# Kernel tuning notes

Hardware: AMD Instinct MI355X
Metric: run time of the kernel (lower is better)

Reference implementation:

```python
import math
import jax, jax.numpy as jnp
import numpy as np

B, T = 4, 160000
D, H, DH, FF, L = 768, 12, 64, 3072, 12
NB, MD = 320, 800  # rel-pos buckets / max distance
CONV = [(1,512,10,5),(512,512,3,2),(512,512,3,2),(512,512,3,2),(512,512,3,2),(512,512,2,2),(512,512,2,2)]
STRIDES = [5,2,2,2,2,2,2]

def _frames(t):
    for _,_,k,s in CONV:
        t = (t - k)//s + 1
    return t
S = _frames(T)  # 499


def setup_inputs() -> dict:
    key = jax.random.key(0)
    ks = iter(jax.random.split(key, 64))
    r = lambda *sh: jax.random.normal(next(ks), sh, jnp.float32) * 0.02
    return {
        "source": jax.random.normal(next(ks), (B, T), jnp.float32),
        "conv_w0": r(512,1,10),
        "conv_w14": r(4,512,512,3),
        "conv_w56": r(2,512,512,2),
        "conv_ln_g": jnp.ones((7,512), jnp.float32), "conv_ln_b": jnp.zeros((7,512), jnp.float32),
        "feat_ln_g": jnp.ones((512,), jnp.float32), "feat_ln_b": jnp.zeros((512,), jnp.float32),
        "proj_w": r(D,512), "proj_b": jnp.zeros((D,), jnp.float32),
        "pos_conv_w": r(D, D//16, 128), "pos_conv_b": jnp.zeros((D,), jnp.float32),
        "enc_ln_g": jnp.ones((D,), jnp.float32), "enc_ln_b": jnp.zeros((D,), jnp.float32),
        "Wq": r(L,D,D), "bq": jnp.zeros((L,D), jnp.float32),
        "Wk": r(L,D,D), "bk": jnp.zeros((L,D), jnp.float32),
        "Wv": r(L,D,D), "bv": jnp.zeros((L,D), jnp.float32),
        "Wo": r(L,D,D), "bo": jnp.zeros((L,D), jnp.float32),
        "grep_w": r(L,8,DH), "grep_b": jnp.zeros((L,8), jnp.float32),
        "grep_a": jnp.ones((L,H), jnp.float32),
        "ln1_g": jnp.ones((L,D), jnp.float32), "ln1_b": jnp.zeros((L,D), jnp.float32),
        "fc1_w": r(L,FF,D), "fc1_b": jnp.zeros((L,FF), jnp.float32),
        "fc2_w": r(L,D,FF), "fc2_b": jnp.zeros((L,D), jnp.float32),
        "ln2_g": jnp.ones((L,D), jnp.float32), "ln2_b": jnp.zeros((L,D), jnp.float32),
        "rel_emb": r(NB,H),
    }


def _ln(x, g, b, eps=1e-5):
    m = jnp.mean(x, -1, keepdims=True)
    v = jnp.mean((x - m) ** 2, -1, keepdims=True)
    return (x - m) * jax.lax.rsqrt(v + eps) * g + b


def _conv1d(x, w, stride, pad=0, groups=1):
    return jax.lax.conv_general_dilated(x, w, (stride,), [(pad, pad)],
        dimension_numbers=('NCH', 'OIH', 'NCH'), feature_group_count=groups)


def _buckets(s):
    # T5-style bidirectional relative-position bucketization (WavLM compute_bias)
    rel = jnp.arange(s)[None, :] - jnp.arange(s)[:, None]  # memory - context
    nb = NB // 2
    b = (rel > 0).astype(jnp.int32) * nb
    n = jnp.abs(rel)
    max_exact = nb // 2
    large = max_exact + (jnp.log(jnp.maximum(n, 1).astype(jnp.float32) / max_exact)
                         / math.log(MD / max_exact) * (nb - max_exact)).astype(jnp.int32)
    large = jnp.minimum(large, nb - 1)
    return b + jnp.where(n < max_exact, n, large)


def _fwd(p):
    # ---- conv feature extractor: (B,T) -> (B,512,S)
    x = p["source"][:, None, :]
    ws = [p["conv_w0"]] + [p["conv_w14"][i] for i in range(4)] + [p["conv_w56"][i] for i in range(2)]
    for i, (w, st) in enumerate(zip(ws, STRIDES)):
        x = _conv1d(x, w, st)
        x = _ln(x.transpose(0, 2, 1), p["conv_ln_g"][i], p["conv_ln_b"][i]).transpose(0, 2, 1)
        x = jax.nn.gelu(x, approximate=False)
    x = x.transpose(0, 2, 1)                       # (B,S,512)
    x = _ln(x, p["feat_ln_g"], p["feat_ln_b"])
    x = x @ p["proj_w"].T + p["proj_b"]            # (B,S,768) post_extract_proj
    # ---- positional conv (kernel 128, pad 64, groups 16, SamePad drops last)
    xc = _conv1d(x.transpose(0, 2, 1), p["pos_conv_w"], 1, pad=64, groups=16) + p["pos_conv_b"][None, :, None]
    xc = jax.nn.gelu(xc[:, :, :-1], approximate=False)
    x = x + xc.transpose(0, 2, 1)
    x = _ln(x, p["enc_ln_g"], p["enc_ln_b"])       # layer_norm_first=False -> LN before layers
    Bn, s, _ = x.shape
    pos_bias = p["rel_emb"][_buckets(s)].transpose(2, 0, 1)  # (H,S,S), computed at layer 0, reused
    scaling = DH ** -0.5
    for l in range(L):
        # gated relative-position bias: gates from raw layer-input split into heads (WavLM fast path)
        ql = x.reshape(Bn, s, H, DH).transpose(0, 2, 1, 3)        # (B,H,S,dh)
        g = jax.nn.sigmoid((jnp.einsum('bhsd,gd->bhsg', ql, p["grep_w"][l]) + p["grep_b"][l])
                           .reshape(Bn, H, s, 2, 4).sum(-1))       # (B,H,S,2)
        gate = g[..., 0] * (g[..., 1] * p["grep_a"][l][None, :, None] - 1.0) + 2.0  # (B,H,S)
        bias = gate[..., None] * pos_bias[None]                    # (B,H,S,S)
        def proj(W, bb):
            return (x @ W.T + bb).reshape(Bn, s, H, DH).transpose(0, 2, 1, 3)
        q = proj(p["Wq"][l], p["bq"][l]) * scaling
        k = proj(p["Wk"][l], p["bk"][l])
        v = proj(p["Wv"][l], p["bv"][l])
        attn = jax.nn.softmax(jnp.einsum('bhsd,bhtd->bhst', q, k) + bias, axis=-1)
        ctx = jnp.einsum('bhst,bhtd->bhsd', attn, v).transpose(0, 2, 1, 3).reshape(Bn, s, D)
        x = _ln(x + ctx @ p["Wo"][l].T + p["bo"][l], p["ln1_g"][l], p["ln1_b"][l])
        h = jax.nn.gelu(x @ p["fc1_w"][l].T + p["fc1_b"][l], approximate=False)
        x = _ln(x + h @ p["fc2_w"][l].T + p["fc2_b"][l], p["ln2_g"][l], p["ln2_b"][l])
    return x


def reference(source, conv_w0, conv_w14, conv_w56, conv_ln_g, conv_ln_b, feat_ln_g, feat_ln_b,
              proj_w, proj_b, pos_conv_w, pos_conv_b, enc_ln_g, enc_ln_b,
              Wq, bq, Wk, bk, Wv, bv, Wo, bo, grep_w, grep_b, grep_a,
              ln1_g, ln1_b, fc1_w, fc1_b, fc2_w, fc2_b, ln2_g, ln2_b, rel_emb):
    p = dict(source=source, conv_w0=conv_w0, conv_w14=conv_w14, conv_w56=conv_w56,
             conv_ln_g=conv_ln_g, conv_ln_b=conv_ln_b, feat_ln_g=feat_ln_g, feat_ln_b=feat_ln_b,
             proj_w=proj_w, proj_b=proj_b, pos_conv_w=pos_conv_w, pos_conv_b=pos_conv_b,
             enc_ln_g=enc_ln_g, enc_ln_b=enc_ln_b, Wq=Wq, bq=bq, Wk=Wk, bk=bk, Wv=Wv, bv=bv,
             Wo=Wo, bo=bo, grep_w=grep_w, grep_b=grep_b, grep_a=grep_a,
             ln1_g=ln1_g, ln1_b=ln1_b, fc1_w=fc1_w, fc1_b=fc1_b, fc2_w=fc2_w, fc2_b=fc2_b,
             ln2_g=ln2_g, ln2_b=ln2_b, rel_emb=rel_emb)
    return _fwd(p)
```

## Files before the change

kernel.cpp:

```cpp
#include <hip/hip_runtime.h>
#include <hip/hip_bf16.h>
#include <math.h>

namespace {

constexpr int BATCH  = 4;
constexpr int T_IN   = 160000;
constexpr int DMODEL = 768;
constexpr int NHEAD  = 12;
constexpr int DHEAD  = 64;
constexpr int FFN    = 3072;
constexpr int NLAYER = 12;
constexpr int SEQ    = 499;
constexpr int SP     = 512;
constexpr int NREL   = 2 * SEQ - 1;

typedef __hip_bfloat16 bf16;
using f32x4 = __attribute__((ext_vector_type(4))) float;
using s16x8 = __attribute__((ext_vector_type(8))) short;

__device__ __forceinline__ float gelu_f(float x){
  return 0.5f * x * (1.0f + erff(x * 0.70710678118654752f));
}

__device__ __forceinline__ unsigned f2bf_rne(float f){
  unsigned u = __float_as_uint(f);
  return (u + 0x7FFFu + ((u >> 16) & 1u)) >> 16;
}

__global__ void fill_f32_kernel(float* __restrict__ out, int n, float val){
  int i = blockIdx.x * 256 + threadIdx.x;
  if (i < n) out[i] = val;
}

__global__ void f2bf_kernel(const float* __restrict__ in, bf16* __restrict__ out, int n){
  int i = blockIdx.x * 256 + threadIdx.x;
  if (i < n) out[i] = __float2bfloat16(in[i]);
}

__global__ void castw6(const float* __restrict__ wq, const float* __restrict__ wk,
                       const float* __restrict__ wv, const float* __restrict__ wo,
                       const float* __restrict__ f1, const float* __restrict__ f2,
                       bf16* __restrict__ d0, bf16* __restrict__ d1, bf16* __restrict__ d2,
                       bf16* __restrict__ d3, bf16* __restrict__ d4, bf16* __restrict__ d5){
  int z = blockIdx.y;
  int idx = blockIdx.x * 256 + threadIdx.x;
  const float* s; bf16* d; int n;
  switch (z){
    case 0: s = wq; d = d0; n = 589824; break;
    case 1: s = wk; d = d1; n = 589824; break;
    case 2: s = wv; d = d2; n = 589824; break;
    case 3: s = wo; d = d3; n = 589824; break;
    case 4: s = f1; d = d4; n = 2359296; break;
    default: s = f2; d = d5; n = 2359296; break;
  }
  if (idx < n) d[idx] = __float2bfloat16(s[idx]);
}

template<int KW>
__global__ void pack_convw(const float* __restrict__ w, bf16* __restrict__ dst){
  int idx = blockIdx.x * 256 + threadIdx.x;
  if (idx >= KW * 512 * 512) return;
  int ci = idx & 511, co = (idx >> 9) & 511, k = idx >> 18;
  dst[idx] = __float2bfloat16(w[((size_t)co * 512 + ci) * KW + k]);
}

__global__ void conv0_kernel(const float* __restrict__ src, const float* __restrict__ w,
                             float* __restrict__ out, int Lout){
  int idx = blockIdx.x * 256 + threadIdx.x;
  if (idx >= 512 * Lout) return;
  int c = idx / Lout, t = idx - c * Lout;
  const float* wr = w + c * 10;
  const float* s  = src + t * 5;
  float acc = 0.f;
#pragma unroll
  for (int k = 0; k < 10; k++) acc += wr[k] * s[k];
  out[idx] = acc;
}

template<int BFOUT>
__global__ void ln_gelu_ch2_kernel(float* __restrict__ x, bf16* __restrict__ ob,
                                   const float* __restrict__ g, const float* __restrict__ b,
                                   int Lt){
  const int tid = threadIdx.x;
  const int tt = tid & 31, tc = tid >> 5;
  const int t = blockIdx.x * 32 + tt;
  __shared__ float sred[8][33], qred[8][33];
  __shared__ float mrow[32], rrow[32];
  float s = 0.f, q = 0.f;
  if (t < Lt){
    const float* xc = x + (size_t)(tc * 64) * Lt + t;
#pragma unroll 8
    for (int j = 0; j < 64; j++){ float v = xc[(size_t)j * Lt]; s += v; q += v * v; }
  }
  sred[tc][tt] = s; qred[tc][tt] = q; __syncthreads();
  if (tid < 32){
    float ss = 0.f, qq = 0.f;
#pragma unroll
    for (int c = 0; c < 8; c++){ ss += sred[c][tid]; qq += qred[c][tid]; }
    float m = ss * (1.f / 512.f);
    float var = qq * (1.f / 512.f) - m * m;
    mrow[tid] = m; rrow[tid] = rsqrtf(var + 1e-5f);
  }
  __syncthreads();
  if (t < Lt){
    float m = mrow[tt], rs = rrow[tt];
    float* xc = x + (size_t)(tc * 64) * Lt + t;
#pragma unroll 8
    for (int j = 0; j < 64; j++){
      int c = tc * 64 + j;
      float v = gelu_f((xc[(size_t)j * Lt] - m) * rs * g[c] + b[c]);
      if (BFOUT) ob[(size_t)c * Lt + t] = __float2bfloat16(v);
      else       xc[(size_t)j * Lt] = v;
    }
  }
}

template<int KW>
__global__ void conv_mfma_kernel(const bf16* __restrict__ in, const bf16* __restrict__ wpk,
                                 float* __restrict__ out, int Lin, int Lout, int outLd){
  __shared__ unsigned comb[130][33];
  __shared__ bf16 As[KW][64][40];
  const int tid = threadIdx.x, wid = tid >> 6, lane = tid & 63;
  const int co0 = blockIdx.x * 64, t0 = blockIdx.y * 128;
  const int wm = (wid >> 1) * 32, wn = (wid & 1) * 64;
  const int fr = lane & 15, fk = (lane >> 4) * 8;
  const int wco = tid >> 2, wci = (tid & 3) * 8;
  f32x4 acc[2][4] = {};
  for (int ci0 = 0; ci0 < 512; ci0 += 32){
#pragma unroll
    for (int k = 0; k < KW; k++)
      *reinterpret_cast<uint4*>(&As[k][wco][wci]) =
        *reinterpret_cast<const uint4*>(&wpk[(size_t)k * 262144 + (size_t)(co0 + wco) * 512 + ci0 + wci]);
    for (int idx = tid; idx < 4096; idx += 256){
      int jp = idx & 127, ci = idx >> 7;
      int gp = t0 * 2 + 2 * jp;
      const bf16* rp = in + (size_t)(ci0 + ci) * Lin;
      unsigned pr = 0;
      if (gp + 1 < Lin) pr = *reinterpret_cast<const unsigned*>(&rp[gp]);
      else if (gp < Lin) pr = *reinterpret_cast<const unsigned short*>(&rp[gp]);
      comb[jp][ci] = pr;
    }
    if (tid < 64){
      int jp = 128 + (tid >> 5), ci = tid & 31;
      int gp = t0 * 2 + 2 * jp;
      const bf16* rp = in + (size_t)(ci0 + ci) * Lin;
      unsigned pr = 0;
      if (gp + 1 < Lin) pr = *reinterpret_cast<const unsigned*>(&rp[gp]);
      else if (gp < Lin) pr = *reinterpret_cast<const unsigned short*>(&rp[gp]);
      comb[jp][ci] = pr;
    }
    __syncthreads();
#pragma unroll
    for (int k = 0; k < KW; k++){
      const int ro = k >> 1, par = k & 1;
      s16x8 a0 = *reinterpret_cast<const s16x8*>(&As[k][wm + fr][fk]);
      s16x8 a1 = *reinterpret_cast<const s16x8*>(&As[k][wm + 16 + fr][fk]);
#pragma unroll
      for (int ni = 0; ni < 4; ni++){
        const unsigned* cp = &comb[wn + ni * 16 + fr + ro][fk];
        unsigned u0 = cp[0], u1 = cp[1], u2 = cp[2], u3 = cp[3];
        unsigned u4 = cp[4], u5 = cp[5], u6 = cp[6], u7 = cp[7];
        uint4 pb;
        if (par){
          pb.x = (u0 >> 16) | (u1 & 0xFFFF0000u);
          pb.y = (u2 >> 16) | (u3 & 0xFFFF0000u);
          pb.z = (u4 >> 16) | (u5 & 0xFFFF0000u);
          pb.w = (u6 >> 16) | (u7 & 0xFFFF0000u);
        } else {
          pb.x = (u0 & 0xFFFFu) | (u1 << 16);
          pb.y = (u2 & 0xFFFFu) | (u3 << 16);
          pb.z = (u4 & 0xFFFFu) | (u5 << 16);
          pb.w = (u6 & 0xFFFFu) | (u7 << 16);
        }
        s16x8 bb = *reinterpret_cast<s16x8*>(&pb);
        acc[0][ni] = __builtin_amdgcn_mfma_f32_16x16x32_bf16(a0, bb, acc[0][ni], 0, 0, 0);
        acc[1][ni] = __builtin_amdgcn_mfma_f32_16x16x32_bf16(a1, bb, acc[1][ni], 0, 0, 0);
      }
    }
    __syncthreads();
  }
  const int cc = lane & 15, crr = (lane >> 4) * 4;
#pragma unroll
  for (int mi = 0; mi < 2; mi++){
#pragma unroll
    for (int ni = 0; ni < 4; ni++){
      int t = t0 + wn + ni * 16 + cc;
      if (t >= Lout) continue;
#pragma unroll
      for (int r = 0; r < 4; r++){
        int co = co0 + wm + mi * 16 + crr + r;
        out[(size_t)co * outLd + t] = acc[mi][ni][r];
      }
    }
  }
}

__global__ void featln_transpose_kernel(const float* __restrict__ xin,
                                        const float* __restrict__ g, const float* __restrict__ b,
                                        float* __restrict__ feat){
  int t = blockIdx.x * 256 + threadIdx.x;
  if (t >= SEQ) return;
  float s = 0.f, sq = 0.f;
  for (int c = 0; c < 512; c++){ float v = xin[c * SEQ + t]; s += v; sq += v * v; }
  float m = s * (1.f / 512.f), var = sq * (1.f / 512.f) - m * m, rs = rsqrtf(var + 1e-5f);
  for (int c = 0; c < 512; c++)
    feat[t * 512 + c] = (xin[c * SEQ + t] - m) * rs * g[c] + b[c];
}

template<int ACT>
__global__ void gemm_mfma_f32(const float* __restrict__ A, const float* __restrict__ W,
                              const float* __restrict__ bias, float* __restrict__ C,
                              int M, int N, int K, float alpha){
  __shared__ bf16 As[64][40];
  __shared__ bf16 Ws[64][40];
  const int tid = threadIdx.x;
  const int wid = tid >> 6, lane = tid & 63;
  const int m0 = blockIdx.y * 64, n0 = blockIdx.x * 64;
  const int wm = (wid >> 1) * 32, wn = (wid & 1) * 32;
  const int lrow = tid >> 2;
  const int lk   = (tid & 3) * 8;
  const int fr = lane & 15, fk = (lane >> 4) * 8;
  f32x4 acc[2][2] = {};
  for (int k0 = 0; k0 < K; k0 += 32){
    float4 a0 = make_float4(0.f,0.f,0.f,0.f), a1 = make_float4(0.f,0.f,0.f,0.f);
    int gm = m0 + lrow;
    if (gm < M){
      const float* ap = &A[(size_t)gm * K + k0 + lk];
      a0 = *reinterpret_cast<const float4*>(ap);
      a1 = *reinterpret_cast<const float4*>(ap + 4);
    }
    uint4 pa;
    pa.x = f2bf_rne(a0.x) | (f2bf_rne(a0.y) << 16);
    pa.y = f2bf_rne(a0.z) | (f2bf_rne(a0.w) << 16);
    pa.z = f2bf_rne(a1.x) | (f2bf_rne(a1.y) << 16);
    pa.w = f2bf_rne(a1.z) | (f2bf_rne(a1.w) << 16);
    *reinterpret_cast<uint4*>(&As[lrow][lk]) = pa;
    const float* wp = &W[(size_t)(n0 + lrow) * K + k0 + lk];
    float4 w0 = *reinterpret_cast<const float4*>(wp);
    float4 w1 = *reinterpret_cast<const float4*>(wp + 4);
    uint4 pw;
    pw.x = f2bf_rne(w0.x) | (f2bf_rne(w0.y) << 16);
    pw.y = f2bf_rne(w0.z) | (f2bf_rne(w0.w) << 16);
    pw.z = f2bf_rne(w1.x) | (f2bf_rne(w1.y) << 16);
    pw.w = f2bf_rne(w1.z) | (f2bf_rne(w1.w) << 16);
    *reinterpret_cast<uint4*>(&Ws[lrow][lk]) = pw;
    __syncthreads();
    s16x8 av0 = *reinterpret_cast<const s16x8*>(&As[wm + fr][fk]);
    s16x8 av1 = *reinterpret_cast<const s16x8*>(&As[wm + 16 + fr][fk]);
    s16x8 bv0 = *reinterpret_cast<const s16x8*>(&Ws[wn + fr][fk]);
    s16x8 bv1 = *reinterpret_cast<const s16x8*>(&Ws[wn + 16 + fr][fk]);
    acc[0][0] = __builtin_amdgcn_mfma_f32_16x16x32_bf16(av0, bv0, acc[0][0], 0, 0, 0);
    acc[0][1] = __builtin_amdgcn_mfma_f32_16x16x32_bf16(av0, bv1, acc[0][1], 0, 0, 0);
    acc[1][0] = __builtin_amdgcn_mfma_f32_16x16x32_bf16(av1, bv0, acc[1][0], 0, 0, 0);
    acc[1][1] = __builtin_amdgcn_mfma_f32_16x16x32_bf16(av1, bv1, acc[1][1], 0, 0, 0);
    __syncthreads();
  }
  const int cc = lane & 15, cr = (lane >> 4) * 4;
#pragma unroll
  for (int mi = 0; mi < 2; mi++){
#pragma unroll
    for (int ni = 0; ni < 2; ni++){
      int n = n0 + wn + ni * 16 + cc;
      float bn = bias[n];
#pragma unroll
      for (int r = 0; r < 4; r++){
        int m = m0 + wm + mi * 16 + cr + r;
        if (m < M){
          float v = alpha * (acc[mi][ni][r] + bn);
          if (ACT == 1) v = gelu_f(v);
          C[(size_t)m * N + n] = v;
        }
      }
    }
  }
}

template<int ACT, int OUTBF>
__global__ void gemm_bf(const bf16* __restrict__ A, const bf16* __restrict__ W,
                        const float* __restrict__ bias, void* __restrict__ Cp,
                        int M, int N, int K, float alpha){
  __shared__ bf16 As[64][72];
  __shared__ bf16 Ws[64][72];
  const int tid = threadIdx.x, wid = tid >> 6, lane = tid & 63;
  const int m0 = blockIdx.y * 64, n0 = blockIdx.x * 64;
  const int wm = (wid >> 1) * 32, wn = (wid & 1) * 32;
  const int lrow = tid >> 2, lcol = (tid & 3) * 16;
  const int fr = lane & 15, fk = (lane >> 4) * 8;
  f32x4 acc[2][2] = {};
  for (int k0 = 0; k0 < K; k0 += 64){
    uint4 a0 = make_uint4(0,0,0,0), a1 = make_uint4(0,0,0,0);
    if (m0 + lrow < M){
      const bf16* ap = &A[(size_t)(m0 + lrow) * K + k0 + lcol];
      a0 = *reinterpret_cast<const uint4*>(ap);
      a1 = *reinterpret_cast<const uint4*>(ap + 8);
    }
    *reinterpret_cast<uint4*>(&As[lrow][lcol])     = a0;
    *reinterpret_cast<uint4*>(&As[lrow][lcol + 8]) = a1;
    const bf16* wp = &W[(size_t)(n0 + lrow) * K + k0 + lcol];
    *reinterpret_cast<uint4*>(&Ws[lrow][lcol])     = *reinterpret_cast<const uint4*>(wp);
    *reinterpret_cast<uint4*>(&Ws[lrow][lcol + 8]) = *reinterpret_cast<const uint4*>(wp + 8);
    __syncthreads();
#pragma unroll
    for (int kk = 0; kk < 2; kk++){
      const int c = kk * 32 + fk;
      s16x8 av0 = *reinterpret_cast<const s16x8*>(&As[wm + fr][c]);
      s16x8 av1 = *reinterpret_cast<const s16x8*>(&As[wm + 16 + fr][c]);
      s16x8 bv0 = *reinterpret_cast<const s16x8*>(&Ws[wn + fr][c]);
      s16x8 bv1 = *reinterpret_cast<const s16x8*>(&Ws[wn + 16 + fr][c]);
      acc[0][0] = __builtin_amdgcn_mfma_f32_16x16x32_bf16(av0, bv0, acc[0][0], 0, 0, 0);
      acc[0][1] = __builtin_amdgcn_mfma_f32_16x16x32_bf16(av0, bv1, acc[0][1], 0, 0, 0);
      acc[1][0] = __builtin_amdgcn_mfma_f32_16x16x32_bf16(av1, bv0, acc[1][0], 0, 0, 0);
      acc[1][1] = __builtin_amdgcn_mfma_f32_16x16x32_bf16(av1, bv1, acc[1][1], 0, 0, 0);
    }
    __syncthreads();
  }
  const int cc = lane & 15, cr = (lane >> 4) * 4;
#pragma unroll
  for (int mi = 0; mi < 2; mi++){
#pragma unroll
    for (int ni = 0; ni < 2; ni++){
      int n = n0 + wn + ni * 16 + cc;
      float bn = bias[n];
#pragma unroll
      for (int r = 0; r < 4; r++){
        int m = m0 + wm + mi * 16 + cr + r;
        if (m < M){
          float v = alpha * (acc[mi][ni][r] + bn);
          if (ACT == 1) v = gelu_f(v);
          if (OUTBF) ((bf16*)Cp)[(size_t)m * N + n] = __float2bfloat16(v);
          else       ((float*)Cp)[(size_t)m * N + n] = v;
        }
      }
    }
  }
}

__global__ void qkv_bf(const bf16* __restrict__ A,
                       const bf16* __restrict__ Wq, const bf16* __restrict__ Wk,
                       const bf16* __restrict__ Wv,
                       const float* __restrict__ bqv, const float* __restrict__ bkv,
                       const float* __restrict__ bvv,
                       bf16* __restrict__ qb, bf16* __restrict__ kb,
                       bf16* __restrict__ vb, int M){
  const int z = blockIdx.z;
  const bf16* W   = (z == 0) ? Wq : (z == 1) ? Wk : Wv;
  const float* bia = (z == 0) ? bqv : (z == 1) ? bkv : bvv;
  bf16* C         = (z == 0) ? qb : (z == 1) ? kb : vb;
  const float alpha = (z == 0) ? 0.125f : 1.0f;
  const int K = DMODEL, N = DMODEL;
  __shared__ bf16 As[64][72];
  __shared__ bf16 Ws[64][72];
  const int tid = threadIdx.x, wid = tid >> 6, lane = tid & 63;
  const int m0 = blockIdx.y * 64, n0 = blockIdx.x * 64;
  const int wm = (wid >> 1) * 32, wn = (wid & 1) * 32;
  const int lrow = tid >> 2, lcol = (tid & 3) * 16;
  const int fr = lane & 15, fk = (lane >> 4) * 8;
  f32x4 acc[2][2] = {};
  for (int k0 = 0; k0 < K; k0 += 64){
    uint4 a0 = make_uint4(0,0,0,0), a1 = make_uint4(0,0,0,0);
    if (m0 + lrow < M){
      const bf16* ap = &A[(size_t)(m0 + lrow) * K + k0 + lcol];
      a0 = *reinterpret_cast<const uint4*>(ap);
      a1 = *reinterpret_cast<const uint4*>(ap + 8);
    }
    *reinterpret_cast<uint4*>(&As[lrow][lcol])     = a0;
    *reinterpret_cast<uint4*>(&As[lrow][lcol + 8]) = a1;
    const bf16* wp = &W[(size_t)(n0 + lrow) * K + k0 + lcol];
    *reinterpret_cast<uint4*>(&Ws[lrow][lcol])     = *reinterpret_cast<const uint4*>(wp);
    *reinterpret_cast<uint4*>(&Ws[lrow][lcol + 8]) = *reinterpret_cast<const uint4*>(wp + 8);
    __syncthreads();
#pragma unroll
    for (int kk = 0; kk < 2; kk++){
      const int c = kk * 32 + fk;
      s16x8 av0 = *reinterpret_cast<const s16x8*>(&As[wm + fr][c]);
      s16x8 av1 = *reinterpret_cast<const s16x8*>(&As[wm + 16 + fr][c]);
      s16x8 bv0 = *reinterpret_cast<const s16x8*>(&Ws[wn + fr][c]);
      s16x8 bv1 = *reinterpret_cast<const s16x8*>(&Ws[wn + 16 + fr][c]);
      acc[0][0] = __builtin_amdgcn_mfma_f32_16x16x32_bf16(av0, bv0, acc[0][0], 0, 0, 0);
      acc[0][1] = __builtin_amdgcn_mfma_f32_16x16x32_bf16(av0, bv1, acc[0][1], 0, 0, 0);
      acc[1][0] = __builtin_amdgcn_mfma_f32_16x16x32_bf16(av1, bv0, acc[1][0], 0, 0, 0);
      acc[1][1] = __builtin_amdgcn_mfma_f32_16x16x32_bf16(av1, bv1, acc[1][1], 0, 0, 0);
    }
    __syncthreads();
  }
  const int cc = lane & 15, cr = (lane >> 4) * 4;
#pragma unroll
  for (int mi = 0; mi < 2; mi++){
#pragma unroll
    for (int ni = 0; ni < 2; ni++){
      int n = n0 + wn + ni * 16 + cc;
      float bn = bia[n];
#pragma unroll
      for (int r = 0; r < 4; r++){
        int m = m0 + wm + mi * 16 + cr + r;
        if (m < M) C[(size_t)m * N + n] = __float2bfloat16(alpha * (acc[mi][ni][r] + bn));
      }
    }
  }
}

__global__ void posconv_mfma(const float* __restrict__ x, const bf16* __restrict__ wpos,
                             const float* __restrict__ bias, float* __restrict__ xc){
  const int t0 = blockIdx.x * 64, g = blockIdx.y, b = blockIdx.z;
  __shared__ bf16 As[64][40];
  __shared__ float xw[224];
  const int tid = threadIdx.x, wid = tid >> 6, lane = tid & 63;
  const int wm = (wid >> 1) * 32, wn = (wid & 1) * 32;
  const int lrow = tid >> 2, lk = (tid & 3) * 8;
  const int fr = lane & 15, fk = (lane >> 4) * 8;
  f32x4 acc[2][2] = {};
  for (int ci = 0; ci < 48; ci++){
    for (int idx = tid; idx < 191; idx += 256){
      int p = t0 - 64 + idx;
      xw[idx] = (p >= 0 && p < SEQ) ? x[((size_t)(b * SEQ + p)) * DMODEL + g * 48 + ci] : 0.f;
    }
    for (int kk = 0; kk < 128; kk += 32){
      uint4 wa = make_uint4(0, 0, 0, 0);
      if (lrow < 48)
        wa = *reinterpret_cast<const uint4*>(&wpos[(size_t)(g * 48 + lrow) * 6144 + ci * 128 + kk + lk]);
      *reinterpret_cast<uint4*>(&As[lrow][lk]) = wa;
      __syncthreads();
      auto bfragp = [&](int tr)->s16x8{
        int base = tr + kk + fk;
        s16x8 r;
#pragma unroll
        for (int j = 0; j < 8; j++) r[j] = (short)f2bf_rne(xw[base + j]);
        return r;
      };
      s16x8 a0 = *reinterpret_cast<const s16x8*>(&As[wm + fr][fk]);
      s16x8 a1 = *reinterpret_cast<const s16x8*>(&As[wm + 16 + fr][fk]);
      s16x8 b0 = bfragp(wn + fr);
      s16x8 b1 = bfragp(wn + 16 + fr);
      acc[0][0] = __builtin_amdgcn_mfma_f32_16x16x32_bf16(a0, b0, acc[0][0], 0, 0, 0);
      acc[0][1] = __builtin_amdgcn_mfma_f32_16x16x32_bf16(a0, b1, acc[0][1], 0, 0, 0);
      acc[1][0] = __builtin_amdgcn_mfma_f32_16x16x32_bf16(a1, b0, acc[1][0], 0, 0, 0);
      acc[1][1] = __builtin_amdgcn_mfma_f32_16x16x32_bf16(a1, b1, acc[1][1], 0, 0, 0);
      __syncthreads();
    }
  }
  const int cc = lane & 15, cr = (lane >> 4) * 4;
#pragma unroll
  for (int mi = 0; mi < 2; mi++){
#pragma unroll
    for (int ni = 0; ni < 2; ni++){
      int t = t0 + wn + ni * 16 + cc;
      if (t >= SEQ) continue;
#pragma unroll
      for (int r = 0; r < 4; r++){
        int cop = wm + mi * 16 + cr + r;
        if (cop < 48){
          int co = g * 48 + cop;
          xc[((size_t)(b * SEQ + t)) * DMODEL + co] = acc[mi][ni][r] + bias[co];
        }
      }
    }
  }
}

__global__ void attn_fused(const bf16* __restrict__ q, const bf16* __restrict__ k,
                           const bf16* __restrict__ v, const float* __restrict__ x,
                           const float* __restrict__ gwl, const float* __restrict__ gbl,
                           const float* __restrict__ gal,
                           const float* __restrict__ tab, bf16* __restrict__ ctx){
  const int bh = blockIdx.y, b = bh / NHEAD, h = bh % NHEAD;
  const int i0 = blockIdx.x * 16;
  const int tid = threadIdx.x, w = tid >> 6, lane = tid & 63;
  const int fr = lane & 15, fk = (lane >> 4) * 8;
  const int cr = (lane >> 4) * 4;
  __shared__ float sc[16][524];
  __shared__ short qs[16][72];
  __shared__ short kv[64][72];
  __shared__ float gtmp[16][9];
  __shared__ float gl[16];
  {
    int r = tid >> 4, c = (tid & 15) * 4;
    int gi = i0 + r;
    uint2 p = make_uint2(0, 0);
    if (gi < SEQ) p = *reinterpret_cast<const uint2*>(&q[((size_t)(b*SEQ+gi))*DMODEL + h*DHEAD + c]);
    *reinterpret_cast<uint2*>(&qs[r][c]) = p;
  }
  if (tid < 128){
    int r = tid >> 3, g = tid & 7;
    int gi = i0 + r;
    float a = gbl[g];
    if (gi < SEQ){
      const float* xv = x + ((size_t)(b * SEQ + gi)) * DMODEL + h * DHEAD;
      const float* wrow = gwl + g * DHEAD;
#pragma unroll
      for (int d = 0; d < 64; d++) a += xv[d] * wrow[d];
    }
    gtmp[r][g] = a;
  }
  __syncthreads();
  if (tid < 16){
    float a0 = gtmp[tid][0] + gtmp[tid][1] + gtmp[tid][2] + gtmp[tid][3];
    float a1 = gtmp[tid][4] + gtmp[tid][5] + gtmp[tid][6] + gtmp[tid][7];
    float g0 = 1.f / (1.f + expf(-a0));
    float g1 = 1.f / (1.f + expf(-a1));
    gl[tid] = g0 * (g1 * gal[h] - 1.f) + 2.f;
  }
  for (int j0 = 0; j0 < SP; j0 += 64){
    __syncthreads();
    {
      int jr = tid >> 2, c0 = (tid & 3) * 16;
      int gj = j0 + jr;
      uint4 p0 = make_uint4(0,0,0,0), p1 = make_uint4(0,0,0,0);
      if (gj < SEQ){
        const bf16* kp = &k[((size_t)(b*SEQ+gj))*DMODEL + h*DHEAD + c0];
        p0 = *reinterpret_cast<const uint4*>(kp);
        p1 = *reinterpret_cast<const uint4*>(kp + 8);
      }
      *reinterpret_cast<uint4*>(&kv[jr][c0])     = p0;
      *reinterpret_cast<uint4*>(&kv[jr][c0 + 8]) = p1;
    }
    __syncthreads();
    f32x4 accqk = {};
#pragma unroll
    for (int kk = 0; kk < 2; kk++){
      s16x8 a = *reinterpret_cast<const s16x8*>(&qs[fr][kk*32 + fk]);
      s16x8 bb = *reinterpret_cast<const s16x8*>(&kv[w*16 + fr][kk*32 + fk]);
      accqk = __builtin_amdgcn_mfma_f32_16x16x32_bf16(a, bb, accqk, 0, 0, 0);
    }
#pragma unroll
    for (int r = 0; r < 4; r++)
      sc[cr + r][j0 + w*16 + fr] = accqk[r];
  }
  __syncthreads();
  for (int r = 0; r < 4; r++){
    int row = w * 4 + r;
    int gi = i0 + row;
    if (gi >= SEQ) continue;
    float gt = gl[row];
    const float* tb = tab + (size_t)h * NREL + (SEQ - 1 - gi);
    float vals[8];
    float mx = -1e30f;
#pragma unroll
    for (int it = 0; it < 8; it++){
      int j = lane + it * 64;
      float vv = (j < SEQ) ? (sc[row][j] + gt * tb[j]) : -1e30f;
      vals[it] = vv; mx = fmaxf(mx, vv);
    }
#pragma unroll
    for (int m = 32; m > 0; m >>= 1) mx = fmaxf(mx, __shfl_xor(mx, m));
    float sum = 0.f;
#pragma unroll
    for (int it = 0; it < 8; it++){
      int j = lane + it * 64;
      float e = (j < SEQ) ? expf(vals[it] - mx) : 0.f;
      vals[it] = e; sum += e;
    }
#pragma unroll
    for (int m = 32; m > 0; m >>= 1) sum += __shfl_xor(sum, m);
    float inv = 1.f / sum;
#pragma unroll
    for (int it = 0; it < 8; it++){
      int j = lane + it * 64;
      sc[row][j] = vals[it] * inv;
    }
  }
  __syncthreads();
  f32x4 accpv = {};
  for (int j0 = 0; j0 < SP; j0 += 64){
    __syncthreads();
    {
      int jr = tid >> 2, c0 = (tid & 3) * 16;
      int gj = j0 + jr;
      uint4 p0 = make_uint4(0,0,0,0), p1 = make_uint4(0,0,0,0);
      if (gj < SEQ){
        const bf16* vp = &v[((size_t)(b*SEQ+gj))*DMODEL + h*DHEAD + c0];
        p0 = *reinterpret_cast<const uint4*>(vp);
        p1 = *reinterpret_cast<const uint4*>(vp + 8);
      }
      *reinterpret_cast<uint4*>(&kv[jr][c0])     = p0;
      *reinterpret_cast<uint4*>(&kv[jr][c0 + 8]) = p1;
    }
    __syncthreads();
#pragma unroll
    for (int kk = 0; kk < 2; kk++){
      s16x8 a, bb;
#pragma unroll
      for (int e = 0; e < 8; e++){
        a[e]  = (short)f2bf_rne(sc[fr][j0 + kk*32 + fk + e]);
        bb[e] = kv[kk*32 + fk + e][w*16 + fr];
      }
      accpv = __builtin_amdgcn_mfma_f32_16x16x32_bf16(a, bb, accpv, 0, 0, 0);
    }
  }
#pragma unroll
  for (int r = 0; r < 4; r++){
    int gi = i0 + cr + r;
    if (gi < SEQ)
      ctx[((size_t)(b*SEQ+gi))*DMODEL + h*DHEAD + w*16 + fr] = __float2bfloat16(accpv[r]);
  }
}

template<int GELU_ADD>
__global__ void add_ln_wave(float* __restrict__ x, const float* __restrict__ add,
                            const float* __restrict__ g, const float* __restrict__ b,
                            bf16* __restrict__ xb){
  int row = blockIdx.x * 4 + (threadIdx.x >> 6);
  if (row >= BATCH * SEQ) return;
  int lane = threadIdx.x & 63;
  float* xr = x + (size_t)row * DMODEL;
  const float* ar = add + (size_t)row * DMODEL;
  float buf[12];
  float s = 0.f;
#pragma unroll
  for (int it = 0; it < 12; it++){
    int i = lane + it * 64;
    float v = ar[i];
    if (GELU_ADD) v = gelu_f(v);
    v += xr[i];
    buf[it] = v; s += v;
  }
#pragma unroll
  for (int m = 32; m > 0; m >>= 1) s += __shfl_xor(s, m);
  float mean = s * (1.f / 768.f);
  float q = 0.f;
#pragma unroll
  for (int it = 0; it < 12; it++){ float d = buf[it] - mean; q += d * d; }
#pragma unroll
  for (int m = 32; m > 0; m >>= 1) q += __shfl_xor(q, m);
  float rs = rsqrtf(q * (1.f / 768.f) + 1e-5f);
#pragma unroll
  for (int it = 0; it < 12; it++){
    int i = lane + it * 64;
    float o = (buf[it] - mean) * rs * g[i] + b[i];
    xr[i] = o;
    xb[(size_t)row * DMODEL + i] = __float2bfloat16(o);
  }
}

__global__ void relbias_kernel(const float* __restrict__ rel_emb, float* __restrict__ tab){
  int idx = blockIdx.x * 256 + threadIdx.x;
  if (idx >= NREL * NHEAD) return;
  int rr = idx / NHEAD, h = idx - rr * NHEAD;
  int rel = rr - (SEQ - 1);
  int bkt = (rel > 0) ? 160 : 0;
  int n = (rel < 0) ? -rel : rel;
  if (n < 80) bkt += n;
  else {
    int large = 80 + (int)(logf((float)n / 80.f) / logf(10.f) * 80.f);
    bkt += (large < 159) ? large : 159;
  }
  tab[h * NREL + rr] = rel_emb[bkt * NHEAD + h];
}

}

extern "C" void kernel_launch(void* const* d_in, const int* in_sizes, int n_in,
                              void* d_out, int out_size, void* d_ws, size_t ws_size,
                              hipStream_t stream){
  (void)ws_size;

  static const int DS[34] = {640000,5120,3145728,1048576,3584,3584,512,512,393216,768,
                             4718592,768,768,768,7077888,9216,7077888,9216,7077888,9216,
                             7077888,9216,6144,96,144,9216,9216,28311552,36864,28311552,
                             9216,9216,9216,3840};
  bool ok = (n_in == 34) && (out_size == BATCH * SEQ * DMODEL);
  if (ok) for (int i = 0; i < 34; i++) if (in_sizes[i] != DS[i]) { ok = false; break; }
  if (!ok){
    fill_f32_kernel<<<(out_size + 255) / 256, 256, 0, stream>>>((float*)d_out, out_size, 1000.0f);
    return;
  }

  const float* src  = (const float*)d_in[0];
  const float* w0   = (const float*)d_in[1];
  const float* w14  = (const float*)d_in[2];
  const float* w56  = (const float*)d_in[3];
  const float* clng = (const float*)d_in[4];
  const float* clnb = (const float*)d_in[5];
  const float* flng = (const float*)d_in[6];
  const float* flnb = (const float*)d_in[7];
  const float* pjw  = (const float*)d_in[8];
  const float* pjb  = (const float*)d_in[9];
  const float* pcw  = (const float*)d_in[10];
  const float* pcb  = (const float*)d_in[11];
  const float* eng  = (const float*)d_in[12];
  const float* enb  = (const float*)d_in[13];
  const float* Wq   = (const float*)d_in[14];
  const float* bq   = (const float*)d_in[15];
  const float* Wk   = (const float*)d_in[16];
  const float* bk   = (const float*)d_in[17];
  const float* Wv   = (const float*)d_in[18];
  const float* bv   = (const float*)d_in[19];
  const float* Wo   = (const float*)d_in[20];
  const float* bo   = (const float*)d_in[21];
  const float* gw   = (const float*)d_in[22];
  const float* gbp  = (const float*)d_in[23];
  const float* ga   = (const float*)d_in[24];
  const float* l1g  = (const float*)d_in[25];
  const float* l1b  = (const float*)d_in[26];
  const float* f1w  = (const float*)d_in[27];
  const float* f1b  = (const float*)d_in[28];
  const float* f2w  = (const float*)d_in[29];
  const float* f2b  = (const float*)d_in[30];
  const float* l2g  = (const float*)d_in[31];
  const float* l2b  = (const float*)d_in[32];
  const float* rel  = (const float*)d_in[33];

  float* x = (float*)d_out;

  float* wsf = (float*)d_ws;
  size_t off = 0;
  auto alloc = [&](size_t n){ float* pp = wsf + off; off += (n + 63) & ~(size_t)63; return pp; };
  constexpr size_t F_N   = (size_t)512 * 31999;
  constexpr size_t BFA_N = (size_t)512 * 31999 / 2 + 32;
  float* U = alloc(F_N + BFA_N);
  float* F  = U;
  bf16* bfA = (bf16*)(U + F_N);
  bf16* bfB = (bf16*)(U + 9000000);
  bf16* ffhb = (bf16*)U;
  float* tmp = U + 3100000;
  bf16* qbb  = (bf16*)(U + 4700000);
  bf16* kbb  = (bf16*)(U + 5500000);
  bf16* vbb  = (bf16*)(U + 6300000);
  bf16* ctxb = (bf16*)(U + 7100000);
  bf16* xb   = (bf16*)(U + 7900000);
  bf16* wposb= (bf16*)(U + 8700000);
  float* feat = alloc((size_t)BATCH * SEQ * 512);
  float* c6   = alloc((size_t)512 * SEQ);
  float* tab  = alloc((size_t)NHEAD * NREL);
  bf16* wpk   = (bf16*)alloc(2097152);
  bf16* wqb  = (bf16*)alloc(294912);
  bf16* wkb  = (bf16*)alloc(294912);
  bf16* wvb  = (bf16*)alloc(294912);
  bf16* wob  = (bf16*)alloc(294912);
  bf16* wf1b = (bf16*)alloc(1179648);
  bf16* wf2b = (bf16*)alloc(1179648);

  const int Ls[8] = {160000, 31999, 15999, 7999, 3999, 1999, 999, 499};
  const int Mrows = BATCH * SEQ;

  size_t wpkOff[7];
  {
    size_t o = 0;
    for (int st = 1; st <= 6; st++){ wpkOff[st] = o; o += (st <= 4 ? 3 : 2) * 262144; }
  }
  for (int st = 1; st <= 4; st++)
    pack_convw<3><<<(3 * 262144 + 255) / 256, 256, 0, stream>>>(
        w14 + (size_t)(st - 1) * 512 * 512 * 3, wpk + wpkOff[st]);
  for (int st = 5; st <= 6; st++)
    pack_convw<2><<<(2 * 262144 + 255) / 256, 256, 0, stream>>>(
        w56 + (size_t)(st - 5) * 512 * 512 * 2, wpk + wpkOff[st]);

  for (int b = 0; b < BATCH; b++){
    conv0_kernel<<<(512 * Ls[1] + 255) / 256, 256, 0, stream>>>(src + (size_t)b * T_IN, w0, F, Ls[1]);
    ln_gelu_ch2_kernel<1><<<(Ls[1] + 31) / 32, 256, 0, stream>>>(F, bfA, clng, clnb, Ls[1]);
    bf16* bfin[2] = {bfA, bfB};
    for (int st = 1; st <= 6; st++){
      const bf16* inb = bfin[(st + 1) & 1];
      int Lin = Ls[st], Lout = Ls[st + 1];
      float* outf = (st == 6) ? c6 : F;
      int oLd = (st == 6) ? SEQ : Lout;
      dim3 grd(8, (Lout + 127) / 128);
      if (st <= 4)
        conv_mfma_kernel<3><<<grd, 256, 0, stream>>>(inb, wpk + wpkOff[st], outf, Lin, Lout, oLd);
      else
        conv_mfma_kernel<2><<<grd, 256, 0, stream>>>(inb, wpk + wpkOff[st], outf, Lin, Lout, oLd);
      if (st < 6)
        ln_gelu_ch2_kernel<1><<<(Lout + 31) / 32, 256, 0, stream>>>(F, bfin[st & 1], clng + st * 512, clnb + st * 512, Lout);
    }
    ln_gelu_ch2_kernel<0><<<(SEQ + 31) / 32, 256, 0, stream>>>(c6, nullptr, clng + 6 * 512, clnb + 6 * 512, SEQ);
    featln_transpose_kernel<<<(SEQ + 255) / 256, 256, 0, stream>>>(c6, flng, flnb, feat + (size_t)b * SEQ * 512);
  }

  gemm_mfma_f32<0><<<dim3(DMODEL / 64, (Mrows + 63) / 64), 256, 0, stream>>>(feat, pjw, pjb, x, Mrows, DMODEL, 512, 1.0f);
  f2bf_kernel<<<(4718592 + 255) / 256, 256, 0, stream>>>(pcw, wposb, 4718592);
  posconv_mfma<<<dim3(8, 16, BATCH), 256, 0, stream>>>(x, wposb, pcb, tmp);
  add_ln_wave<1><<<(Mrows + 3) / 4, 256, 0, stream>>>(x, tmp, eng, enb, xb);
  relbias_kernel<<<(NREL * NHEAD + 255) / 256, 256, 0, stream>>>(rel, tab);

  const size_t WQK = (size_t)DMODEL * DMODEL;
  const size_t WF  = (size_t)FFN * DMODEL;
  for (int l = 0; l < NLAYER; l++){
    castw6<<<dim3(9216, 6), 256, 0, stream>>>(
        Wq + l * WQK, Wk + l * WQK, Wv + l * WQK, Wo + l * WQK,
        f1w + l * WF, f2w + l * WF, wqb, wkb, wvb, wob, wf1b, wf2b);
    qkv_bf<<<dim3(12, 32, 3), 256, 0, stream>>>(
        xb, wqb, wkb, wvb, bq + l * DMODEL, bk + l * DMODEL, bv + l * DMODEL,
        qbb, kbb, vbb, Mrows);
    attn_fused<<<dim3(32, BATCH * NHEAD), 256, 0, stream>>>(
        qbb, kbb, vbb, x, gw + (size_t)l * 8 * DHEAD, gbp + l * 8, ga + l * NHEAD, tab, ctxb);
    gemm_bf<0, 0><<<dim3(12, 32), 256, 0, stream>>>(ctxb, wob, bo + l * DMODEL, tmp, Mrows, DMODEL, DMODEL, 1.0f);
    add_ln_wave<0><<<(Mrows + 3) / 4, 256, 0, stream>>>(x, tmp, l1g + l * DMODEL, l1b + l * DMODEL, xb);
    gemm_bf<1, 1><<<dim3(FFN / 64, 32), 256, 0, stream>>>(xb, wf1b, f1b + l * FFN, ffhb, Mrows, FFN, DMODEL, 1.0f);
    gemm_bf<0, 0><<<dim3(12, 32), 256, 0, stream>>>(ffhb, wf2b, f2b + l * DMODEL, tmp, Mrows, DMODEL, FFN, 1.0f);
    add_ln_wave<0><<<(Mrows + 3) / 4, 256, 0, stream>>>(x, tmp, l2g + l * DMODEL, l2b + l * DMODEL, xb);
  }
}
```

Measured before the change: 5.808 ms.

## Register-prefetch next tiles in conv/GEMM loops and split-K the Wo and FC2 GEMMs

The conv MFMA, gemm_bf and qkv kernels now load the next K-slice from global memory into registers while the current tile is being computed, hiding load latency behind the MFMA work. The Wo and FC2 projections are split into two launches that each cover half of K and write two partial outputs. The residual add+LayerNorm kernel sums both partials. This costs more registers and an extra launch plus a partial buffer per split GEMM. The split-K launches run one after the other on the same stream, so they do not raise concurrency and only shorten each launch's K loop.

```diff
diff --git a/kernel.cpp b/kernel.cpp
--- a/kernel.cpp
+++ b/kernel.cpp
@@ -127,19 +127,22 @@
   const int fr = lane & 15, fk = (lane >> 4) * 8;
   const int wco = tid >> 2, wci = (tid & 3) * 8;
   f32x4 acc[2][4] = {};
-  for (int ci0 = 0; ci0 < 512; ci0 += 32){
+  uint4 rw[KW];
+  unsigned rin[16], rex = 0;
+  auto LOAD = [&](int ci0){
 #pragma unroll
     for (int k = 0; k < KW; k++)
-      *reinterpret_cast<uint4*>(&As[k][wco][wci]) =
-        *reinterpret_cast<const uint4*>(&wpk[(size_t)k * 262144 + (size_t)(co0 + wco) * 512 + ci0 + wci]);
-    for (int idx = tid; idx < 4096; idx += 256){
+      rw[k] = *reinterpret_cast<const uint4*>(&wpk[(size_t)k * 262144 + (size_t)(co0 + wco) * 512 + ci0 + wci]);
+#pragma unroll
+    for (int s = 0; s < 16; s++){
+      int idx = s * 256 + tid;
       int jp = idx & 127, ci = idx >> 7;
       int gp = t0 * 2 + 2 * jp;
       const bf16* rp = in + (size_t)(ci0 + ci) * Lin;
       unsigned pr = 0;
       if (gp + 1 < Lin) pr = *reinterpret_cast<const unsigned*>(&rp[gp]);
       else if (gp < Lin) pr = *reinterpret_cast<const unsigned short*>(&rp[gp]);
-      comb[jp][ci] = pr;
+      rin[s] = pr;
     }
     if (tid < 64){
       int jp = 128 + (tid >> 5), ci = tid & 31;
@@ -148,9 +151,22 @@
       unsigned pr = 0;
       if (gp + 1 < Lin) pr = *reinterpret_cast<const unsigned*>(&rp[gp]);
       else if (gp < Lin) pr = *reinterpret_cast<const unsigned short*>(&rp[gp]);
-      comb[jp][ci] = pr;
-    }
-    __syncthreads();
+      rex = pr;
+    }
+  };
+  LOAD(0);
+  for (int ci0 = 0; ci0 < 512; ci0 += 32){
+#pragma unroll
+    for (int k = 0; k < KW; k++)
+      *reinterpret_cast<uint4*>(&As[k][wco][wci]) = rw[k];
+#pragma unroll
+    for (int s = 0; s < 16; s++){
+      int idx = s * 256 + tid;
+      comb[idx & 127][idx >> 7] = rin[s];
+    }
+    if (tid < 64) comb[128 + (tid >> 5)][tid & 31] = rex;
+    __syncthreads();
+    if (ci0 + 32 < 512) LOAD(ci0 + 32);
 #pragma unroll
     for (int k = 0; k < KW; k++){
       const int ro = k >> 1, par = k & 1;
@@ -279,7 +295,7 @@
 template<int ACT, int OUTBF>
 __global__ void gemm_bf(const bf16* __restrict__ A, const bf16* __restrict__ W,
                         const float* __restrict__ bias, void* __restrict__ Cp,
-                        int M, int N, int K, float alpha){
+                        int M, int N, int K, int kOff, int kLen, float alpha){
   __shared__ bf16 As[64][72];
   __shared__ bf16 Ws[64][72];
   const int tid = threadIdx.x, wid = tid >> 6, lane = tid & 63;
@@ -288,19 +304,26 @@
   const int lrow = tid >> 2, lcol = (tid & 3) * 16;
   const int fr = lane & 15, fk = (lane >> 4) * 8;
   f32x4 acc[2][2] = {};
-  for (int k0 = 0; k0 < K; k0 += 64){
-    uint4 a0 = make_uint4(0,0,0,0), a1 = make_uint4(0,0,0,0);
+  uint4 ra0, ra1, rw0, rw1;
+  auto LOAD = [&](int k0){
+    ra0 = make_uint4(0,0,0,0); ra1 = make_uint4(0,0,0,0);
     if (m0 + lrow < M){
-      const bf16* ap = &A[(size_t)(m0 + lrow) * K + k0 + lcol];
-      a0 = *reinterpret_cast<const uint4*>(ap);
-      a1 = *reinterpret_cast<const uint4*>(ap + 8);
-    }
-    *reinterpret_cast<uint4*>(&As[lrow][lcol])     = a0;
-    *reinterpret_cast<uint4*>(&As[lrow][lcol + 8]) = a1;
-    const bf16* wp = &W[(size_t)(n0 + lrow) * K + k0 + lcol];
-    *reinterpret_cast<uint4*>(&Ws[lrow][lcol])     = *reinterpret_cast<const uint4*>(wp);
-    *reinterpret_cast<uint4*>(&Ws[lrow][lcol + 8]) = *reinterpret_cast<const uint4*>(wp + 8);
-    __syncthreads();
+      const bf16* ap = &A[(size_t)(m0 + lrow) * K + kOff + k0 + lcol];
+      ra0 = *reinterpret_cast<const uint4*>(ap);
+      ra1 = *reinterpret_cast<const uint4*>(ap + 8);
+    }
+    const bf16* wp = &W[(size_t)(n0 + lrow) * K + kOff + k0 + lcol];
+    rw0 = *reinterpret_cast<const uint4*>(wp);
+    rw1 = *reinterpret_cast<const uint4*>(wp + 8);
+  };
+  LOAD(0);
+  for (int k0 = 0; k0 < kLen; k0 += 64){
+    *reinterpret_cast<uint4*>(&As[lrow][lcol])     = ra0;
+    *reinterpret_cast<uint4*>(&As[lrow][lcol + 8]) = ra1;
+    *reinterpret_cast<uint4*>(&Ws[lrow][lcol])     = rw0;
+    *reinterpret_cast<uint4*>(&Ws[lrow][lcol + 8]) = rw1;
+    __syncthreads();
+    if (k0 + 64 < kLen) LOAD(k0 + 64);
 #pragma unroll
     for (int kk = 0; kk < 2; kk++){
       const int c = kk * 32 + fk;
@@ -321,7 +344,7 @@
 #pragma unroll
     for (int ni = 0; ni < 2; ni++){
       int n = n0 + wn + ni * 16 + cc;
-      float bn = bias[n];
+      float bn = bias ? bias[n] : 0.f;
 #pragma unroll
       for (int r = 0; r < 4; r++){
         int m = m0 + wm + mi * 16 + cr + r;
@@ -357,19 +380,26 @@
   const int lrow = tid >> 2, lcol = (tid & 3) * 16;
   const int fr = lane & 15, fk = (lane >> 4) * 8;
   f32x4 acc[2][2] = {};
-  for (int k0 = 0; k0 < K; k0 += 64){
-    uint4 a0 = make_uint4(0,0,0,0), a1 = make_uint4(0,0,0,0);
+  uint4 ra0, ra1, rw0, rw1;
+  auto LOAD = [&](int k0){
+    ra0 = make_uint4(0,0,0,0); ra1 = make_uint4(0,0,0,0);
     if (m0 + lrow < M){
       const bf16* ap = &A[(size_t)(m0 + lrow) * K + k0 + lcol];
-      a0 = *reinterpret_cast<const uint4*>(ap);
-      a1 = *reinterpret_cast<const uint4*>(ap + 8);
-    }
-    *reinterpret_cast<uint4*>(&As[lrow][lcol])     = a0;
-    *reinterpret_cast<uint4*>(&As[lrow][lcol + 8]) = a1;
+      ra0 = *reinterpret_cast<const uint4*>(ap);
+      ra1 = *reinterpret_cast<const uint4*>(ap + 8);
+    }
     const bf16* wp = &W[(size_t)(n0 + lrow) * K + k0 + lcol];
-    *reinterpret_cast<uint4*>(&Ws[lrow][lcol])     = *reinterpret_cast<const uint4*>(wp);
-    *reinterpret_cast<uint4*>(&Ws[lrow][lcol + 8]) = *reinterpret_cast<const uint4*>(wp + 8);
-    __syncthreads();
+    rw0 = *reinterpret_cast<const uint4*>(wp);
+    rw1 = *reinterpret_cast<const uint4*>(wp + 8);
+  };
+  LOAD(0);
+  for (int k0 = 0; k0 < K; k0 += 64){
+    *reinterpret_cast<uint4*>(&As[lrow][lcol])     = ra0;
+    *reinterpret_cast<uint4*>(&As[lrow][lcol + 8]) = ra1;
+    *reinterpret_cast<uint4*>(&Ws[lrow][lcol])     = rw0;
+    *reinterpret_cast<uint4*>(&Ws[lrow][lcol + 8]) = rw1;
+    __syncthreads();
+    if (k0 + 64 < K) LOAD(k0 + 64);
 #pragma unroll
     for (int kk = 0; kk < 2; kk++){
       const int c = kk * 32 + fk;
@@ -595,8 +625,9 @@
   }
 }
 
-template<int GELU_ADD>
+template<int GELU_ADD, int TWO>
 __global__ void add_ln_wave(float* __restrict__ x, const float* __restrict__ add,
+                            const float* __restrict__ add2,
                             const float* __restrict__ g, const float* __restrict__ b,
                             bf16* __restrict__ xb){
   int row = blockIdx.x * 4 + (threadIdx.x >> 6);
@@ -604,12 +635,14 @@
   int lane = threadIdx.x & 63;
   float* xr = x + (size_t)row * DMODEL;
   const float* ar = add + (size_t)row * DMODEL;
+  const float* ar2 = TWO ? add2 + (size_t)row * DMODEL : nullptr;
   float buf[12];
   float s = 0.f;
 #pragma unroll
   for (int it = 0; it < 12; it++){
     int i = lane + it * 64;
     float v = ar[i];
+    if (TWO) v += ar2[i];
     if (GELU_ADD) v = gelu_f(v);
     v += xr[i];
     buf[it] = v; s += v;
@@ -719,6 +752,7 @@
   bf16* ctxb = (bf16*)(U + 7100000);
   bf16* xb   = (bf16*)(U + 7900000);
   bf16* wposb= (bf16*)(U + 8700000);
+  float* tmp2 = U + 11100000;
   float* feat = alloc((size_t)BATCH * SEQ * 512);
   float* c6   = alloc((size_t)512 * SEQ);
   float* tab  = alloc((size_t)NHEAD * NREL);
@@ -769,7 +803,7 @@
   gemm_mfma_f32<0><<<dim3(DMODEL / 64, (Mrows + 63) / 64), 256, 0, stream>>>(feat, pjw, pjb, x, Mrows, DMODEL, 512, 1.0f);
   f2bf_kernel<<<(4718592 + 255) / 256, 256, 0, stream>>>(pcw, wposb, 4718592);
   posconv_mfma<<<dim3(8, 16, BATCH), 256, 0, stream>>>(x, wposb, pcb, tmp);
-  add_ln_wave<1><<<(Mrows + 3) / 4, 256, 0, stream>>>(x, tmp, eng, enb, xb);
+  add_ln_wave<1, 0><<<(Mrows + 3) / 4, 256, 0, stream>>>(x, tmp, nullptr, eng, enb, xb);
   relbias_kernel<<<(NREL * NHEAD + 255) / 256, 256, 0, stream>>>(rel, tab);
 
   const size_t WQK = (size_t)DMODEL * DMODEL;
@@ -783,10 +817,12 @@
         qbb, kbb, vbb, Mrows);
     attn_fused<<<dim3(32, BATCH * NHEAD), 256, 0, stream>>>(
         qbb, kbb, vbb, x, gw + (size_t)l * 8 * DHEAD, gbp + l * 8, ga + l * NHEAD, tab, ctxb);
-    gemm_bf<0, 0><<<dim3(12, 32), 256, 0, stream>>>(ctxb, wob, bo + l * DMODEL, tmp, Mrows, DMODEL, DMODEL, 1.0f);
-    add_ln_wave<0><<<(Mrows + 3) / 4, 256, 0, stream>>>(x, tmp, l1g + l * DMODEL, l1b + l * DMODEL, xb);
-    gemm_bf<1, 1><<<dim3(FFN / 64, 32), 256, 0, stream>>>(xb, wf1b, f1b + l * FFN, ffhb, Mrows, FFN, DMODEL, 1.0f);
-    gemm_bf<0, 0><<<dim3(12, 32), 256, 0, stream>>>(ffhb, wf2b, f2b + l * DMODEL, tmp, Mrows, DMODEL, FFN, 1.0f);
-    add_ln_wave<0><<<(Mrows + 3) / 4, 256, 0, stream>>>(x, tmp, l2g + l * DMODEL, l2b + l * DMODEL, xb);
-  }
-}
+    gemm_bf<0, 0><<<dim3(12, 32), 256, 0, stream>>>(ctxb, wob, bo + l * DMODEL, tmp,  Mrows, DMODEL, DMODEL, 0,   384, 1.0f);
+    gemm_bf<0, 0><<<dim3(12, 32), 256, 0, stream>>>(ctxb, wob, nullptr,         tmp2, Mrows, DMODEL, DMODEL, 384, 384, 1.0f);
+    add_ln_wave<0, 1><<<(Mrows + 3) / 4, 256, 0, stream>>>(x, tmp, tmp2, l1g + l * DMODEL, l1b + l * DMODEL, xb);
+    gemm_bf<1, 1><<<dim3(FFN / 64, 32), 256, 0, stream>>>(xb, wf1b, f1b + l * FFN, ffhb, Mrows, FFN, DMODEL, 0, DMODEL, 1.0f);
+    gemm_bf<0, 0><<<dim3(12, 32), 256, 0, stream>>>(ffhb, wf2b, f2b + l * DMODEL, tmp,  Mrows, DMODEL, FFN, 0,    1536, 1.0f);
+    gemm_bf<0, 0><<<dim3(12, 32), 256, 0, stream>>>(ffhb, wf2b, nullptr,          tmp2, Mrows, DMODEL, FFN, 1536, 1536, 1.0f);
+    add_ln_wave<0, 1><<<(Mrows + 3) / 4, 256, 0, stream>>>(x, tmp, tmp2, l2g + l * DMODEL, l2b + l * DMODEL, xb);
+  }
+}
```

New measurement: 5.045 ms. -13.1%, faster.
